# Kernel tuning notes

Measured on AMD Instinct MI355X. Metric: run time of the kernel, lower is better.

Reference implementation:

```python
import jax, jax.numpy as jnp
import numpy as np
import math

B, T, C = 2, 2048, 1024
H, DK, DV = 16, 64, 64


def setup_inputs() -> dict:
    key = jax.random.key(0)
    ks = jax.random.split(key, 5)
    # randw(*d) = randn(*d) / sqrt(d[-1])
    x = jax.random.normal(ks[0], (B, T, C), dtype=jnp.float32)
    w_q = jax.random.normal(ks[1], (H, DK, C), dtype=jnp.float32) / math.sqrt(C)
    w_k = jax.random.normal(ks[2], (H, DK, C), dtype=jnp.float32) / math.sqrt(C)
    w_v = jax.random.normal(ks[3], (H, DV, C), dtype=jnp.float32) / math.sqrt(C)
    w_o = jax.random.normal(ks[4], (H * DV, C), dtype=jnp.float32) / math.sqrt(C)
    return {"x": x, "w_q": w_q, "w_k": w_k, "w_v": w_v, "w_o": w_o}


def reference(x, w_q, w_k, w_v, w_o):
    # Full prefill: bs_q.first = 0, bs_q.nb = T, causal=True, dropout=0 (eval).
    dk = w_q.shape[1]
    q = jnp.einsum('ntc,hdc->nhtd', x, w_q)  # [B,H,T,DK]
    k = jnp.einsum('ntc,hdc->nhtd', x, w_k)  # [B,H,T,DK]
    v = jnp.einsum('ntc,hdc->nhtd', x, w_v)  # [B,H,T,DV]
    a = jnp.einsum('nhtd,nhsd->nhts', q, k) / jnp.sqrt(jnp.asarray(dk, x.dtype))
    # amm_generator: mask where query_idx < key_idx (strict upper triangle)
    t = a.shape[-1]
    mask = jnp.arange(t)[:, None] < jnp.arange(t)[None, :]  # [T,T] bool
    a = jnp.where(mask[None, None], jnp.asarray(-jnp.inf, a.dtype), a)
    a = jax.nn.softmax(a, axis=-1)
    y = jnp.einsum('nhts,nhsd->nthd', a, v)  # [B,T,H,DV]
    y = y.reshape(y.shape[0], y.shape[1], -1)  # [B,T,H*DV]
    return y @ w_o  # [B,T,C]
```

## Files before the change

### kernel.cpp

```cpp
#include <hip/hip_runtime.h>
#include <hip/hip_bf16.h>

#define B_ 2
#define T_ 2048
#define C_ 1024
#define H_ 16
#define D_ 64

typedef __attribute__((ext_vector_type(8))) short bf16x8;
typedef __attribute__((ext_vector_type(4))) float f32x4;
typedef __attribute__((ext_vector_type(8))) unsigned short u16x8;
typedef __attribute__((ext_vector_type(2))) unsigned int u32x2;
typedef __attribute__((ext_vector_type(4))) unsigned int u32x4;

__device__ __forceinline__ unsigned short bf1(float a) {
    __bf16 x = (__bf16)a;
    return __builtin_bit_cast(unsigned short, x);
}
__device__ __forceinline__ unsigned int pk2(float a, float b) {
    return (unsigned int)bf1(a) | ((unsigned int)bf1(b) << 16);
}
__device__ __forceinline__ float bf2f(unsigned short u) {
    union { unsigned int u; float f; } v; v.u = (unsigned int)u << 16;
    return v.f;
}

__device__ __forceinline__ void gll16(const void* g, void* l) {
    __builtin_amdgcn_global_load_lds(
        (const __attribute__((address_space(1))) unsigned int*)g,
        (__attribute__((address_space(3))) unsigned int*)l, 16, 0, 0);
}

__global__ __launch_bounds__(256) void prep_all(
    const float* __restrict__ x, const float* __restrict__ wq,
    const float* __restrict__ wk, const float* __restrict__ wv,
    unsigned short* __restrict__ xb, unsigned short* __restrict__ wb)
{
    const int bid = blockIdx.x, tid = threadIdx.x;
    if (bid < 1024) {
        const size_t i = ((size_t)bid * 256 + tid) * 16;
        float4 f0 = *reinterpret_cast<const float4*>(x + i);
        float4 f1 = *reinterpret_cast<const float4*>(x + i + 4);
        float4 f2 = *reinterpret_cast<const float4*>(x + i + 8);
        float4 f3 = *reinterpret_cast<const float4*>(x + i + 12);
        u32x4 a = {pk2(f0.x, f0.y), pk2(f0.z, f0.w), pk2(f1.x, f1.y), pk2(f1.z, f1.w)};
        u32x4 b = {pk2(f2.x, f2.y), pk2(f2.z, f2.w), pk2(f3.x, f3.y), pk2(f3.z, f3.w)};
        *reinterpret_cast<u32x4*>(xb + i) = a;
        *reinterpret_cast<u32x4*>(xb + i + 8) = b;
    } else {
        const int rb = (bid - 1024) * 4;
        const float* src = (rb < 1024) ? wq + (size_t)rb * 1024
                         : (rb < 2048) ? wk + (size_t)(rb - 1024) * 1024
                                       : wv + (size_t)(rb - 2048) * 1024;
        const float sc = (rb < 1024) ? 0.125f * 1.4426950408889634f : 1.0f;
        const float4* s4 = (const float4*)src;
        u32x2* d = (u32x2*)(wb + (size_t)rb * 1024);
#pragma unroll
        for (int k = 0; k < 4; k++) {
            float4 v = s4[k * 256 + tid];
            u32x2 w;
            w[0] = pk2(v.x * sc, v.y * sc);
            w[1] = pk2(v.z * sc, v.w * sc);
            d[k * 256 + tid] = w;
        }
    }
}

__global__ __launch_bounds__(256) void qkv_gemm(
    const unsigned short* __restrict__ xb, const unsigned short* __restrict__ wb,
    unsigned short* __restrict__ qkv)
{
    __shared__ __align__(16) unsigned short As[128 * 32];
    __shared__ __align__(16) unsigned short Bs[128 * 32];
    const int tid = threadIdx.x;
    const int lane = tid & 63, wave = tid >> 6;
    const int g = lane >> 4, c16 = lane & 15;
    const int xcd = blockIdx.x & 7, idx = blockIdx.x >> 3;
    const int bm = (xcd << 2) + idx / 24, bn = idx % 24;
    const int jbase = bn << 7;
    const int which = jbase >> 10;

    const int srow = lane >> 2, sch = (lane & 3) << 3;
    const unsigned short* asrc = xb + ((size_t)(bm << 7) + wave * 32 + srow) * C_ + sch;
    const unsigned short* bsrc = wb + ((size_t)(bn << 7) + wave * 32 + srow) * C_ + sch;

    f32x4 acc[4][4];
#pragma unroll
    for (int i = 0; i < 4; i++)
#pragma unroll
        for (int j = 0; j < 4; j++) acc[i][j] = (f32x4){0.f, 0.f, 0.f, 0.f};

    const int wm = (wave >> 1) << 6, wn = (wave & 1) << 6;

    for (int t = 0; t < 32; ++t) {
        const int k0 = t << 5;
        __syncthreads();
        gll16(asrc + k0,           &As[(wave * 32) << 5]);
        gll16(asrc + k0 + 16 * C_, &As[(wave * 32 + 16) << 5]);
        gll16(bsrc + k0,           &Bs[(wave * 32) << 5]);
        gll16(bsrc + k0 + 16 * C_, &Bs[(wave * 32 + 16) << 5]);
        __syncthreads();

        bf16x8 af[4], bfv[4];
#pragma unroll
        for (int m = 0; m < 4; m++)
            af[m] = *reinterpret_cast<const bf16x8*>(&As[((wm + m * 16 + c16) << 5) + g * 8]);
#pragma unroll
        for (int n = 0; n < 4; n++)
            bfv[n] = *reinterpret_cast<const bf16x8*>(&Bs[((wn + n * 16 + c16) << 5) + g * 8]);
#pragma unroll
        for (int m = 0; m < 4; m++)
#pragma unroll
            for (int n = 0; n < 4; n++)
                acc[m][n] = __builtin_amdgcn_mfma_f32_16x16x32_bf16(af[m], bfv[n], acc[m][n], 0, 0, 0);
    }

    if (which < 2) {
#pragma unroll
        for (int m = 0; m < 4; m++) {
            const int grow = (bm << 7) + wm + m * 16 + (g << 2);
#pragma unroll
            for (int n = 0; n < 4; n++) {
                const int jj = (jbase + wn + n * 16 + c16) & 1023;
                const int h = jj >> 6, d = jj & 63;
#pragma unroll
                for (int r = 0; r < 4; r++) {
                    const int row = grow + r;
                    const int b = row >> 11, t = row & 2047;
                    const size_t off = ((size_t)((which * B_ + b) * H_ + h) * T_ + t) * 64 + d;
                    qkv[off] = bf1(acc[m][n][r]);
                }
            }
        }
    } else {
#pragma unroll
        for (int m = 0; m < 4; m++) {
            const int grow = (bm << 7) + wm + m * 16 + (g << 2);
            const int b = grow >> 11, t = grow & 2047;
#pragma unroll
            for (int n = 0; n < 4; n++) {
                const int jj = (jbase + wn + n * 16 + c16) & 1023;
                const int h = jj >> 6, d = jj & 63;
                u32x2 w;
                w[0] = pk2(acc[m][n][0], acc[m][n][1]);
                w[1] = pk2(acc[m][n][2], acc[m][n][3]);
                const size_t off = ((size_t)((2 * B_ + b) * H_ + h) * 64 + d) * T_ + t;
                *reinterpret_cast<u32x2*>(&qkv[off]) = w;
            }
        }
    }
}

__global__ __launch_bounds__(256) void attn(
    const unsigned short* __restrict__ qkv,
    unsigned short* __restrict__ opA, unsigned short* __restrict__ opB,
    float* __restrict__ lbuf)
{
    __shared__ __align__(16) unsigned short Ks0[64 * 64], Ks1[64 * 64];
    __shared__ __align__(16) unsigned short Vt0[64 * 64], Vt1[64 * 64];
    __shared__ __align__(16) unsigned short Ps[4][16 * 64];
    const int tid = threadIdx.x, lane = tid & 63, wave = tid >> 6;
    const int g = lane >> 4, c16 = lane & 15;
    const int xs = blockIdx.x & 7;
    const int inner = blockIdx.x >> 3;
    const int qt = 15 - (inner >> 3);
    const int split = (inner >> 2) & 1;
    const int bh = (xs << 2) + (inner & 3);
    const int b = bh >> 4, h = bh & 15;
    const size_t headoff = (size_t)(b * H_ + h) * T_ * 64;
    const size_t QSZ = (size_t)B_ * H_ * T_ * 64;
    const unsigned short* qp = qkv + headoff;
    const unsigned short* kp = qkv + QSZ + headoff;
    const unsigned short* vTp = qkv + 2 * QSZ + headoff;

    const int h1 = qt + 1;
    const int itlo = split ? h1 : 0, ithi = split ? (2 * qt + 2) : h1;

    const int qb0 = (qt << 7) + wave * 16;
    const int qb1 = qb0 + 64;
    bf16x8 qf00, qf01, qf10, qf11;
    {
        const size_t r0 = (size_t)(qb0 + c16) * 64;
        const size_t r1 = (size_t)(qb1 + c16) * 64;
        qf00 = *reinterpret_cast<const bf16x8*>(qp + r0 + g * 8);
        qf01 = *reinterpret_cast<const bf16x8*>(qp + r0 + 32 + g * 8);
        qf10 = *reinterpret_cast<const bf16x8*>(qp + r1 + g * 8);
        qf11 = *reinterpret_cast<const bf16x8*>(qp + r1 + 32 + g * 8);
    }

    const bf16x8 ones = {0x3F80, 0x3F80, 0x3F80, 0x3F80, 0x3F80, 0x3F80, 0x3F80, 0x3F80};
    f32x4 lac0 = (f32x4){0.f, 0.f, 0.f, 0.f}, lac1 = (f32x4){0.f, 0.f, 0.f, 0.f};
    f32x4 acc0[4], acc1[4];
#pragma unroll
    for (int i = 0; i < 4; i++) {
        acc0[i] = (f32x4){0.f, 0.f, 0.f, 0.f};
        acc1[i] = (f32x4){0.f, 0.f, 0.f, 0.f};
    }

    const int sw = c16 & 7;
    const int rdo0 = (c16 << 6) + ((g ^ sw) << 3);
    const int rdo1 = (c16 << 6) + (((g + 4) ^ sw) << 3);
    const unsigned short* krA0 = Ks0 + rdo0;
    const unsigned short* krA1 = Ks0 + rdo1;
    const unsigned short* krB0 = Ks1 + rdo0;
    const unsigned short* krB1 = Ks1 + rdo1;
    const unsigned short* vrA0 = Vt0 + rdo0;
    const unsigned short* vrA1 = Vt0 + rdo1;
    const unsigned short* vrB0 = Vt1 + rdo0;
    const unsigned short* vrB1 = Vt1 + rdo1;
    const unsigned short* par0 = Ps[wave] + rdo0;
    const unsigned short* par1 = Ps[wave] + rdo1;
    unsigned short* pw[4];
#pragma unroll
    for (int f = 0; f < 4; f++)
        pw[f] = Ps[wave] + (c16 << 6)
              + (((((f << 1) + (g >> 1))) ^ sw) << 3) + ((g & 1) << 2);

    const int srow8 = lane >> 3;
    const int swc = ((lane & 7) ^ srow8) << 3;
    const unsigned short* ksrc = kp + (size_t)(wave * 16 + srow8) * 64 + swc;
    const unsigned short* vsrc = vTp + (size_t)(wave * 16 + srow8) * T_ + swc;

    auto stageTo = [&](unsigned short* kd, unsigned short* vd, int s0) {
#pragma unroll
        for (int i = 0; i < 2; i++) {
            gll16(ksrc + (size_t)(s0 + i * 8) * 64, kd + ((wave * 16 + i * 8) << 6));
            gll16(vsrc + s0 + (size_t)i * 8 * T_, vd + ((wave * 16 + i * 8) << 6));
        }
    };

    auto body = [&](const unsigned short* kr0, const unsigned short* kr1,
                    const unsigned short* vr0, const unsigned short* vr1, int s0) {
        f32x4 s0f[4], s1f[4];
#pragma unroll
        for (int f = 0; f < 4; f++) {
            s0f[f] = (f32x4){-16.f, -16.f, -16.f, -16.f};
            s1f[f] = (f32x4){-16.f, -16.f, -16.f, -16.f};
        }
        __builtin_amdgcn_s_setprio(1);
#pragma unroll
        for (int f = 0; f < 4; f++) {
            bf16x8 k0 = *reinterpret_cast<const bf16x8*>(kr0 + f * 1024);
            bf16x8 k1 = *reinterpret_cast<const bf16x8*>(kr1 + f * 1024);
            s0f[f] = __builtin_amdgcn_mfma_f32_16x16x32_bf16(k0, qf00, s0f[f], 0, 0, 0);
            s1f[f] = __builtin_amdgcn_mfma_f32_16x16x32_bf16(k0, qf10, s1f[f], 0, 0, 0);
            s0f[f] = __builtin_amdgcn_mfma_f32_16x16x32_bf16(k1, qf01, s0f[f], 0, 0, 0);
            s1f[f] = __builtin_amdgcn_mfma_f32_16x16x32_bf16(k1, qf11, s1f[f], 0, 0, 0);
        }
        __builtin_amdgcn_s_setprio(0);

        if (s0 + 63 > qb0) {
            const int qg = qb0 + c16;
#pragma unroll
            for (int f = 0; f < 4; f++)
#pragma unroll
                for (int r = 0; r < 4; r++)
                    if (s0 + f * 16 + g * 4 + r > qg) s0f[f][r] = -1e30f;
        }
        if (s0 + 63 > qb1) {
            const int qg = qb1 + c16;
#pragma unroll
            for (int f = 0; f < 4; f++)
#pragma unroll
                for (int r = 0; r < 4; r++)
                    if (s0 + f * 16 + g * 4 + r > qg) s1f[f][r] = -1e30f;
        }

        if (s0 <= qb0 + 15) {
#pragma unroll
            for (int f = 0; f < 4; f++)
#pragma unroll
                for (int r = 0; r < 4; r++)
                    s0f[f][r] = __builtin_amdgcn_exp2f(s0f[f][r]);
#pragma unroll
            for (int f = 0; f < 4; f++) {
                u32x2 w;
                w[0] = pk2(s0f[f][0], s0f[f][1]);
                w[1] = pk2(s0f[f][2], s0f[f][3]);
                *reinterpret_cast<u32x2*>(pw[f]) = w;
            }
            __builtin_amdgcn_s_setprio(1);
#pragma unroll
            for (int ks = 0; ks < 2; ks++) {
                bf16x8 pa = *reinterpret_cast<const bf16x8*>(ks ? par1 : par0);
                const unsigned short* vp = ks ? vr1 : vr0;
                lac0 = __builtin_amdgcn_mfma_f32_16x16x32_bf16(ones, pa, lac0, 0, 0, 0);
#pragma unroll
                for (int fd = 0; fd < 4; fd++) {
                    bf16x8 vf = *reinterpret_cast<const bf16x8*>(vp + fd * 1024);
                    acc0[fd] = __builtin_amdgcn_mfma_f32_16x16x32_bf16(vf, pa, acc0[fd], 0, 0, 0);
                }
            }
            __builtin_amdgcn_s_setprio(0);
        }

        {
#pragma unroll
            for (int f = 0; f < 4; f++)
#pragma unroll
                for (int r = 0; r < 4; r++)
                    s1f[f][r] = __builtin_amdgcn_exp2f(s1f[f][r]);
#pragma unroll
            for (int f = 0; f < 4; f++) {
                u32x2 w;
                w[0] = pk2(s1f[f][0], s1f[f][1]);
                w[1] = pk2(s1f[f][2], s1f[f][3]);
                *reinterpret_cast<u32x2*>(pw[f]) = w;
            }
            __builtin_amdgcn_s_setprio(1);
#pragma unroll
            for (int ks = 0; ks < 2; ks++) {
                bf16x8 pa = *reinterpret_cast<const bf16x8*>(ks ? par1 : par0);
                const unsigned short* vp = ks ? vr1 : vr0;
                lac1 = __builtin_amdgcn_mfma_f32_16x16x32_bf16(ones, pa, lac1, 0, 0, 0);
#pragma unroll
                for (int fd = 0; fd < 4; fd++) {
                    bf16x8 vf = *reinterpret_cast<const bf16x8*>(vp + fd * 1024);
                    acc1[fd] = __builtin_amdgcn_mfma_f32_16x16x32_bf16(vf, pa, acc1[fd], 0, 0, 0);
                }
            }
            __builtin_amdgcn_s_setprio(0);
        }
    };

    if (itlo < ithi) {
        stageTo(Ks0, Vt0, itlo << 6);
        int it = itlo;
        while (it + 2 <= ithi) {
            __syncthreads();
            stageTo(Ks1, Vt1, (it + 1) << 6);
            body(krA0, krA1, vrA0, vrA1, it << 6);
            __syncthreads();
            if (it + 2 < ithi) stageTo(Ks0, Vt0, (it + 2) << 6);
            body(krB0, krB1, vrB0, vrB1, (it + 1) << 6);
            it += 2;
        }
        if (it < ithi) {
            __syncthreads();
            body(krA0, krA1, vrA0, vrA1, it << 6);
        }
    }

    unsigned short* op = split ? opB : opA;
#pragma unroll
    for (int fd = 0; fd < 4; fd++) {
        u32x2 w0, w1;
        w0[0] = pk2(acc0[fd][0], acc0[fd][1]);
        w0[1] = pk2(acc0[fd][2], acc0[fd][3]);
        w1[0] = pk2(acc1[fd][0], acc1[fd][1]);
        w1[1] = pk2(acc1[fd][2], acc1[fd][3]);
        const size_t c0 = ((size_t)b * T_ + qb0 + c16) * 1024 + h * 64 + fd * 16 + g * 4;
        const size_t c1 = ((size_t)b * T_ + qb1 + c16) * 1024 + h * 64 + fd * 16 + g * 4;
        *reinterpret_cast<u32x2*>(&op[c0]) = w0;
        *reinterpret_cast<u32x2*>(&op[c1]) = w1;
    }
    if (lane < 16) {
        const size_t base = (size_t)split * (B_ * H_ * T_) + ((size_t)(b * H_ + h)) * T_;
        lbuf[base + qb0 + c16] = lac0[0];
        lbuf[base + qb1 + c16] = lac1[0];
    }
}

__global__ __launch_bounds__(256) void combine_wo(
    const unsigned short* __restrict__ opA, const unsigned short* __restrict__ opB,
    const float* __restrict__ lbuf, unsigned short* __restrict__ y,
    const float* __restrict__ wo, unsigned short* __restrict__ wt)
{
    __shared__ unsigned short tile[64][72];
    const int bid = blockIdx.x, tid = threadIdx.x;
    if (bid < 2048) {
        const size_t i = ((size_t)bid * 256 + tid) * 8;
        const int hh = (int)((i >> 6) & 15);
        const int t = (int)((i >> 10) & 2047);
        const int bb = (int)(i >> 21);
        const size_t li = ((size_t)(bb * H_ + hh)) * T_ + t;
        const float inv = 1.0f / (lbuf[li] + lbuf[(size_t)B_ * H_ * T_ + li]);
        u16x8 a = *reinterpret_cast<const u16x8*>(opA + i);
        u16x8 c = *reinterpret_cast<const u16x8*>(opB + i);
        unsigned short o[8];
#pragma unroll
        for (int j = 0; j < 8; j++) o[j] = bf1((bf2f(a[j]) + bf2f(c[j])) * inv);
        *reinterpret_cast<u16x8*>(y + i) = *reinterpret_cast<u16x8*>(o);
    } else {
        const int wb2 = bid - 2048;
        const int tk = (wb2 & 15) << 6, tn = (wb2 >> 4) << 6;
        const int r = tid >> 2, cb = (tid & 3) << 4;
#pragma unroll
        for (int j = 0; j < 4; j++) {
            float4 v = *reinterpret_cast<const float4*>(
                wo + (size_t)(tk + r) * 1024 + tn + cb + j * 4);
            u32x2 w;
            w[0] = pk2(v.x, v.y);
            w[1] = pk2(v.z, v.w);
            *reinterpret_cast<u32x2*>(&tile[r][cb + j * 4]) = w;
        }
        __syncthreads();
        unsigned short buf[16];
#pragma unroll
        for (int j = 0; j < 16; j++) buf[j] = tile[cb + j][r];
        unsigned short* dst = wt + (size_t)(tn + r) * 1024 + tk + cb;
        *reinterpret_cast<u16x8*>(dst) = *reinterpret_cast<u16x8*>(buf);
        *reinterpret_cast<u16x8*>(dst + 8) = *reinterpret_cast<u16x8*>(buf + 8);
    }
}

__global__ __launch_bounds__(256) void out_proj(
    const unsigned short* __restrict__ y, const unsigned short* __restrict__ wt,
    float* __restrict__ out)
{
    __shared__ __align__(16) unsigned short As[128 * 32];
    __shared__ __align__(16) unsigned short Bs[64 * 32];
    const int tid = threadIdx.x;
    const int lane = tid & 63, wave = tid >> 6;
    const int g = lane >> 4, c16 = lane & 15;
    const int xcd = blockIdx.x & 7, idx = blockIdx.x >> 3;
    const int bm = (xcd << 2) + (idx >> 4), bn = idx & 15;
    const int wm = (wave >> 1) << 6, wn = (wave & 1) << 5;

    const int srow = lane >> 2, sch = (lane & 3) << 3;
    const unsigned short* ysrc = y + ((size_t)(bm << 7) + wave * 32 + srow) * 1024 + sch;
    const unsigned short* wsrc = wt + ((size_t)(bn << 6) + wave * 16 + srow) * 1024 + sch;

    f32x4 acc[4][2];
#pragma unroll
    for (int i = 0; i < 4; i++)
#pragma unroll
        for (int j = 0; j < 2; j++) acc[i][j] = (f32x4){0.f, 0.f, 0.f, 0.f};

    for (int t = 0; t < 32; ++t) {
        const int k0 = t << 5;
        __syncthreads();
        gll16(ysrc + k0,             &As[(wave * 32) << 5]);
        gll16(ysrc + k0 + 16 * 1024, &As[(wave * 32 + 16) << 5]);
        gll16(wsrc + k0,             &Bs[(wave * 16) << 5]);
        __syncthreads();

        bf16x8 af[4], bfr[2];
#pragma unroll
        for (int m = 0; m < 4; m++)
            af[m] = *reinterpret_cast<const bf16x8*>(&As[((wm + m * 16 + c16) << 5) + g * 8]);
#pragma unroll
        for (int n = 0; n < 2; n++)
            bfr[n] = *reinterpret_cast<const bf16x8*>(&Bs[((wn + n * 16 + c16) << 5) + g * 8]);
#pragma unroll
        for (int m = 0; m < 4; m++)
#pragma unroll
            for (int n = 0; n < 2; n++)
                acc[m][n] = __builtin_amdgcn_mfma_f32_16x16x32_bf16(af[m], bfr[n], acc[m][n], 0, 0, 0);
    }

#pragma unroll
    for (int m = 0; m < 4; m++) {
        const int grow = (bm << 7) + wm + m * 16 + (g << 2);
#pragma unroll
        for (int n = 0; n < 2; n++) {
            const int gcol = (bn << 6) + wn + n * 16 + c16;
#pragma unroll
            for (int r = 0; r < 4; r++)
                out[(size_t)(grow + r) * 1024 + gcol] = acc[m][n][r];
        }
    }
}

extern "C" void kernel_launch(void* const* d_in, const int* in_sizes, int n_in,
                              void* d_out, int out_size, void* d_ws, size_t ws_size,
                              hipStream_t stream) {
    const float* x  = (const float*)d_in[0];
    const float* wq = (const float*)d_in[1];
    const float* wk = (const float*)d_in[2];
    const float* wv = (const float*)d_in[3];
    const float* wo = (const float*)d_in[4];
    float* out = (float*)d_out;

    unsigned short* wb   = (unsigned short*)d_ws;
    unsigned short* opB  = (unsigned short*)d_ws;
    unsigned short* y    = opB;
    unsigned short* qkv  = (unsigned short*)d_ws + (size_t)4 * 1024 * 1024;
    unsigned short* wt   = qkv;
    unsigned short* xb   = (unsigned short*)d_out;
    unsigned short* opA  = (unsigned short*)d_out;
    float* lbuf = (float*)((char*)d_out + (size_t)8 * 1024 * 1024);

    prep_all<<<dim3(1792), 256, 0, stream>>>(x, wq, wk, wv, xb, wb);
    qkv_gemm<<<dim3(768), 256, 0, stream>>>(xb, wb, qkv);
    attn<<<dim3(1024), 256, 0, stream>>>(qkv, opA, opB, lbuf);
    combine_wo<<<dim3(2048 + 256), 256, 0, stream>>>(opA, opB, lbuf, y, wo, wt);
    out_proj<<<dim3(512), 256, 0, stream>>>(y, wt, out);
}
```

Before: 108.5 us.

## Pair mirrored 64-row query tiles per block to balance causal attention work

```diff
diff --git a/kernel.cpp b/kernel.cpp
--- a/kernel.cpp
+++ b/kernel.cpp
@@ -163,7 +163,7 @@
     const int g = lane >> 4, c16 = lane & 15;
     const int xs = blockIdx.x & 7;
     const int inner = blockIdx.x >> 3;
-    const int qt = 15 - (inner >> 3);
+    const int p = inner >> 3;
     const int split = (inner >> 2) & 1;
     const int bh = (xs << 2) + (inner & 3);
     const int b = bh >> 4, h = bh & 15;
@@ -173,28 +173,30 @@
     const unsigned short* kp = qkv + QSZ + headoff;
     const unsigned short* vTp = qkv + 2 * QSZ + headoff;
 
-    const int h1 = qt + 1;
-    const int itlo = split ? h1 : 0, ithi = split ? (2 * qt + 2) : h1;
-
-    const int qb0 = (qt << 7) + wave * 16;
-    const int qb1 = qb0 + 64;
-    bf16x8 qf00, qf01, qf10, qf11;
+    const int tA = p, tB = 31 - p;
+    const int hs = (p >= 7) ? 8 : (15 - p);
+    const int itlo = split ? hs : 0;
+    const int ithi = split ? (tB + 1) : hs;
+
+    const int qbA = (tA << 6) + wave * 16;
+    const int qbB = (tB << 6) + wave * 16;
+    bf16x8 qfA0, qfA1, qfB0, qfB1;
     {
-        const size_t r0 = (size_t)(qb0 + c16) * 64;
-        const size_t r1 = (size_t)(qb1 + c16) * 64;
-        qf00 = *reinterpret_cast<const bf16x8*>(qp + r0 + g * 8);
-        qf01 = *reinterpret_cast<const bf16x8*>(qp + r0 + 32 + g * 8);
-        qf10 = *reinterpret_cast<const bf16x8*>(qp + r1 + g * 8);
-        qf11 = *reinterpret_cast<const bf16x8*>(qp + r1 + 32 + g * 8);
+        const size_t rA = (size_t)(qbA + c16) * 64;
+        const size_t rB = (size_t)(qbB + c16) * 64;
+        qfA0 = *reinterpret_cast<const bf16x8*>(qp + rA + g * 8);
+        qfA1 = *reinterpret_cast<const bf16x8*>(qp + rA + 32 + g * 8);
+        qfB0 = *reinterpret_cast<const bf16x8*>(qp + rB + g * 8);
+        qfB1 = *reinterpret_cast<const bf16x8*>(qp + rB + 32 + g * 8);
     }
 
     const bf16x8 ones = {0x3F80, 0x3F80, 0x3F80, 0x3F80, 0x3F80, 0x3F80, 0x3F80, 0x3F80};
-    f32x4 lac0 = (f32x4){0.f, 0.f, 0.f, 0.f}, lac1 = (f32x4){0.f, 0.f, 0.f, 0.f};
-    f32x4 acc0[4], acc1[4];
+    f32x4 lacA = (f32x4){0.f, 0.f, 0.f, 0.f}, lacB = (f32x4){0.f, 0.f, 0.f, 0.f};
+    f32x4 accA[4], accB[4];
 #pragma unroll
     for (int i = 0; i < 4; i++) {
-        acc0[i] = (f32x4){0.f, 0.f, 0.f, 0.f};
-        acc1[i] = (f32x4){0.f, 0.f, 0.f, 0.f};
+        accA[i] = (f32x4){0.f, 0.f, 0.f, 0.f};
+        accB[i] = (f32x4){0.f, 0.f, 0.f, 0.f};
     }
 
     const int sw = c16 & 7;
@@ -230,53 +232,83 @@
     };
 
     auto body = [&](const unsigned short* kr0, const unsigned short* kr1,
-                    const unsigned short* vr0, const unsigned short* vr1, int s0) {
-        f32x4 s0f[4], s1f[4];
+                    const unsigned short* vr0, const unsigned short* vr1, int it) {
+        const int s0 = it << 6;
+        const bool doA = (it <= tA);
+        f32x4 sA[4], sB[4];
 #pragma unroll
         for (int f = 0; f < 4; f++) {
-            s0f[f] = (f32x4){-16.f, -16.f, -16.f, -16.f};
-            s1f[f] = (f32x4){-16.f, -16.f, -16.f, -16.f};
+            sA[f] = (f32x4){-16.f, -16.f, -16.f, -16.f};
+            sB[f] = (f32x4){-16.f, -16.f, -16.f, -16.f};
         }
         __builtin_amdgcn_s_setprio(1);
 #pragma unroll
         for (int f = 0; f < 4; f++) {
             bf16x8 k0 = *reinterpret_cast<const bf16x8*>(kr0 + f * 1024);
             bf16x8 k1 = *reinterpret_cast<const bf16x8*>(kr1 + f * 1024);
-            s0f[f] = __builtin_amdgcn_mfma_f32_16x16x32_bf16(k0, qf00, s0f[f], 0, 0, 0);
-            s1f[f] = __builtin_amdgcn_mfma_f32_16x16x32_bf16(k0, qf10, s1f[f], 0, 0, 0);
-            s0f[f] = __builtin_amdgcn_mfma_f32_16x16x32_bf16(k1, qf01, s0f[f], 0, 0, 0);
-            s1f[f] = __builtin_amdgcn_mfma_f32_16x16x32_bf16(k1, qf11, s1f[f], 0, 0, 0);
+            sB[f] = __builtin_amdgcn_mfma_f32_16x16x32_bf16(k0, qfB0, sB[f], 0, 0, 0);
+            sB[f] = __builtin_amdgcn_mfma_f32_16x16x32_bf16(k1, qfB1, sB[f], 0, 0, 0);
+            if (doA) {
+                sA[f] = __builtin_amdgcn_mfma_f32_16x16x32_bf16(k0, qfA0, sA[f], 0, 0, 0);
+                sA[f] = __builtin_amdgcn_mfma_f32_16x16x32_bf16(k1, qfA1, sA[f], 0, 0, 0);
+            }
         }
         __builtin_amdgcn_s_setprio(0);
 
-        if (s0 + 63 > qb0) {
-            const int qg = qb0 + c16;
+        if (it == tB) {
+            const int qg = qbB + c16;
 #pragma unroll
             for (int f = 0; f < 4; f++)
 #pragma unroll
                 for (int r = 0; r < 4; r++)
-                    if (s0 + f * 16 + g * 4 + r > qg) s0f[f][r] = -1e30f;
-        }
-        if (s0 + 63 > qb1) {
-            const int qg = qb1 + c16;
+                    if (s0 + f * 16 + g * 4 + r > qg) sB[f][r] = -1e30f;
+        }
+
+#pragma unroll
+        for (int f = 0; f < 4; f++)
+#pragma unroll
+            for (int r = 0; r < 4; r++)
+                sB[f][r] = __builtin_amdgcn_exp2f(sB[f][r]);
+#pragma unroll
+        for (int f = 0; f < 4; f++) {
+            u32x2 w;
+            w[0] = pk2(sB[f][0], sB[f][1]);
+            w[1] = pk2(sB[f][2], sB[f][3]);
+            *reinterpret_cast<u32x2*>(pw[f]) = w;
+        }
+        __builtin_amdgcn_s_setprio(1);
+#pragma unroll
+        for (int ks = 0; ks < 2; ks++) {
+            bf16x8 pa = *reinterpret_cast<const bf16x8*>(ks ? par1 : par0);
+            const unsigned short* vp = ks ? vr1 : vr0;
+            lacB = __builtin_amdgcn_mfma_f32_16x16x32_bf16(ones, pa, lacB, 0, 0, 0);
+#pragma unroll
+            for (int fd = 0; fd < 4; fd++) {
+                bf16x8 vf = *reinterpret_cast<const bf16x8*>(vp + fd * 1024);
+                accB[fd] = __builtin_amdgcn_mfma_f32_16x16x32_bf16(vf, pa, accB[fd], 0, 0, 0);
+            }
+        }
+        __builtin_amdgcn_s_setprio(0);
+
+        if (doA) {
+            if (it == tA) {
+                const int qg = qbA + c16;
+#pragma unroll
+                for (int f = 0; f < 4; f++)
+#pragma unroll
+                    for (int r = 0; r < 4; r++)
+                        if (s0 + f * 16 + g * 4 + r > qg) sA[f][r] = -1e30f;
+            }
 #pragma unroll
             for (int f = 0; f < 4; f++)
 #pragma unroll
                 for (int r = 0; r < 4; r++)
-                    if (s0 + f * 16 + g * 4 + r > qg) s1f[f][r] = -1e30f;
-        }
-
-        if (s0 <= qb0 + 15) {
-#pragma unroll
-            for (int f = 0; f < 4; f++)
-#pragma unroll
-                for (int r = 0; r < 4; r++)
-                    s0f[f][r] = __builtin_amdgcn_exp2f(s0f[f][r]);
+                    sA[f][r] = __builtin_amdgcn_exp2f(sA[f][r]);
 #pragma unroll
             for (int f = 0; f < 4; f++) {
                 u32x2 w;
-                w[0] = pk2(s0f[f][0], s0f[f][1]);
-                w[1] = pk2(s0f[f][2], s0f[f][3]);
+                w[0] = pk2(sA[f][0], sA[f][1]);
+                w[1] = pk2(sA[f][2], sA[f][3]);
                 *reinterpret_cast<u32x2*>(pw[f]) = w;
             }
             __builtin_amdgcn_s_setprio(1);
@@ -284,39 +316,11 @@
             for (int ks = 0; ks < 2; ks++) {
                 bf16x8 pa = *reinterpret_cast<const bf16x8*>(ks ? par1 : par0);
                 const unsigned short* vp = ks ? vr1 : vr0;
-                lac0 = __builtin_amdgcn_mfma_f32_16x16x32_bf16(ones, pa, lac0, 0, 0, 0);
+                lacA = __builtin_amdgcn_mfma_f32_16x16x32_bf16(ones, pa, lacA, 0, 0, 0);
 #pragma unroll
                 for (int fd = 0; fd < 4; fd++) {
                     bf16x8 vf = *reinterpret_cast<const bf16x8*>(vp + fd * 1024);
-                    acc0[fd] = __builtin_amdgcn_mfma_f32_16x16x32_bf16(vf, pa, acc0[fd], 0, 0, 0);
-                }
-            }
-            __builtin_amdgcn_s_setprio(0);
-        }
-
-        {
-#pragma unroll
-            for (int f = 0; f < 4; f++)
-#pragma unroll
-                for (int r = 0; r < 4; r++)
-                    s1f[f][r] = __builtin_amdgcn_exp2f(s1f[f][r]);
-#pragma unroll
-            for (int f = 0; f < 4; f++) {
-                u32x2 w;
-                w[0] = pk2(s1f[f][0], s1f[f][1]);
-                w[1] = pk2(s1f[f][2], s1f[f][3]);
-                *reinterpret_cast<u32x2*>(pw[f]) = w;
-            }
-            __builtin_amdgcn_s_setprio(1);
-#pragma unroll
-            for (int ks = 0; ks < 2; ks++) {
-                bf16x8 pa = *reinterpret_cast<const bf16x8*>(ks ? par1 : par0);
-                const unsigned short* vp = ks ? vr1 : vr0;
-                lac1 = __builtin_amdgcn_mfma_f32_16x16x32_bf16(ones, pa, lac1, 0, 0, 0);
-#pragma unroll
-                for (int fd = 0; fd < 4; fd++) {
-                    bf16x8 vf = *reinterpret_cast<const bf16x8*>(vp + fd * 1024);
-                    acc1[fd] = __builtin_amdgcn_mfma_f32_16x16x32_bf16(vf, pa, acc1[fd], 0, 0, 0);
+                    accA[fd] = __builtin_amdgcn_mfma_f32_16x16x32_bf16(vf, pa, accA[fd], 0, 0, 0);
                 }
             }
             __builtin_amdgcn_s_setprio(0);
@@ -329,35 +333,35 @@
         while (it + 2 <= ithi) {
             __syncthreads();
             stageTo(Ks1, Vt1, (it + 1) << 6);
-            body(krA0, krA1, vrA0, vrA1, it << 6);
+            body(krA0, krA1, vrA0, vrA1, it);
             __syncthreads();
             if (it + 2 < ithi) stageTo(Ks0, Vt0, (it + 2) << 6);
-            body(krB0, krB1, vrB0, vrB1, (it + 1) << 6);
+            body(krB0, krB1, vrB0, vrB1, it + 1);
             it += 2;
         }
         if (it < ithi) {
             __syncthreads();
-            body(krA0, krA1, vrA0, vrA1, it << 6);
+            body(krA0, krA1, vrA0, vrA1, it);
         }
     }
 
     unsigned short* op = split ? opB : opA;
 #pragma unroll
     for (int fd = 0; fd < 4; fd++) {
-        u32x2 w0, w1;
-        w0[0] = pk2(acc0[fd][0], acc0[fd][1]);
-        w0[1] = pk2(acc0[fd][2], acc0[fd][3]);
-        w1[0] = pk2(acc1[fd][0], acc1[fd][1]);
-        w1[1] = pk2(acc1[fd][2], acc1[fd][3]);
-        const size_t c0 = ((size_t)b * T_ + qb0 + c16) * 1024 + h * 64 + fd * 16 + g * 4;
-        const size_t c1 = ((size_t)b * T_ + qb1 + c16) * 1024 + h * 64 + fd * 16 + g * 4;
-        *reinterpret_cast<u32x2*>(&op[c0]) = w0;
-        *reinterpret_cast<u32x2*>(&op[c1]) = w1;
+        u32x2 wA, wB;
+        wA[0] = pk2(accA[fd][0], accA[fd][1]);
+        wA[1] = pk2(accA[fd][2], accA[fd][3]);
+        wB[0] = pk2(accB[fd][0], accB[fd][1]);
+        wB[1] = pk2(accB[fd][2], accB[fd][3]);
+        const size_t cA = ((size_t)b * T_ + qbA + c16) * 1024 + h * 64 + fd * 16 + g * 4;
+        const size_t cB = ((size_t)b * T_ + qbB + c16) * 1024 + h * 64 + fd * 16 + g * 4;
+        *reinterpret_cast<u32x2*>(&op[cA]) = wA;
+        *reinterpret_cast<u32x2*>(&op[cB]) = wB;
     }
     if (lane < 16) {
         const size_t base = (size_t)split * (B_ * H_ * T_) + ((size_t)(b * H_ + h)) * T_;
-        lbuf[base + qb0 + c16] = lac0[0];
-        lbuf[base + qb1 + c16] = lac1[0];
+        lbuf[base + qbA + c16] = lacA[0];
+        lbuf[base + qbB + c16] = lacB[0];
     }
 }
 
```

Result: slower. 112.8 us (+4.0%).

## Triple-buffer LDS staging with explicit vmcnt waits in QKV GEMM and attention

Applied to the files above, without the earlier changes.

```diff
diff --git a/kernel.cpp b/kernel.cpp
--- a/kernel.cpp
+++ b/kernel.cpp
@@ -30,6 +30,9 @@
         (const __attribute__((address_space(1))) unsigned int*)g,
         (__attribute__((address_space(3))) unsigned int*)l, 16, 0, 0);
 }
+
+#define VM_WAIT4() asm volatile("s_waitcnt vmcnt(4)" ::: "memory")
+#define VM_WAIT0() asm volatile("s_waitcnt vmcnt(0)" ::: "memory")
 
 __global__ __launch_bounds__(256) void prep_all(
     const float* __restrict__ x, const float* __restrict__ wq,
@@ -70,8 +73,7 @@
     const unsigned short* __restrict__ xb, const unsigned short* __restrict__ wb,
     unsigned short* __restrict__ qkv)
 {
-    __shared__ __align__(16) unsigned short As[128 * 32];
-    __shared__ __align__(16) unsigned short Bs[128 * 32];
+    __shared__ __align__(16) unsigned short ABs[3][2][128 * 32];
     const int tid = threadIdx.x;
     const int lane = tid & 63, wave = tid >> 6;
     const int g = lane >> 4, c16 = lane & 15;
@@ -92,27 +94,36 @@
 
     const int wm = (wave >> 1) << 6, wn = (wave & 1) << 6;
 
+    auto stage = [&](int bi, int k0) {
+        gll16(asrc + k0,           &ABs[bi][0][(wave * 32) << 5]);
+        gll16(asrc + k0 + 16 * C_, &ABs[bi][0][(wave * 32 + 16) << 5]);
+        gll16(bsrc + k0,           &ABs[bi][1][(wave * 32) << 5]);
+        gll16(bsrc + k0 + 16 * C_, &ABs[bi][1][(wave * 32 + 16) << 5]);
+    };
+
+    stage(0, 0);
+    stage(1, 32);
+    int bi = 0;
     for (int t = 0; t < 32; ++t) {
-        const int k0 = t << 5;
-        __syncthreads();
-        gll16(asrc + k0,           &As[(wave * 32) << 5]);
-        gll16(asrc + k0 + 16 * C_, &As[(wave * 32 + 16) << 5]);
-        gll16(bsrc + k0,           &Bs[(wave * 32) << 5]);
-        gll16(bsrc + k0 + 16 * C_, &Bs[(wave * 32 + 16) << 5]);
-        __syncthreads();
-
+        if (t < 31) { VM_WAIT4(); } else { VM_WAIT0(); }
+        __builtin_amdgcn_s_barrier();
+        if (t + 2 < 32) stage(bi + 2 >= 3 ? bi - 1 : bi + 2, (t + 2) << 5);
+
+        const unsigned short* Ab = &ABs[bi][0][0];
+        const unsigned short* Bb = &ABs[bi][1][0];
         bf16x8 af[4], bfv[4];
 #pragma unroll
         for (int m = 0; m < 4; m++)
-            af[m] = *reinterpret_cast<const bf16x8*>(&As[((wm + m * 16 + c16) << 5) + g * 8]);
+            af[m] = *reinterpret_cast<const bf16x8*>(&Ab[((wm + m * 16 + c16) << 5) + g * 8]);
 #pragma unroll
         for (int n = 0; n < 4; n++)
-            bfv[n] = *reinterpret_cast<const bf16x8*>(&Bs[((wn + n * 16 + c16) << 5) + g * 8]);
+            bfv[n] = *reinterpret_cast<const bf16x8*>(&Bb[((wn + n * 16 + c16) << 5) + g * 8]);
 #pragma unroll
         for (int m = 0; m < 4; m++)
 #pragma unroll
             for (int n = 0; n < 4; n++)
                 acc[m][n] = __builtin_amdgcn_mfma_f32_16x16x32_bf16(af[m], bfv[n], acc[m][n], 0, 0, 0);
+        bi = (bi + 1 == 3) ? 0 : bi + 1;
     }
 
     if (which < 2) {
@@ -156,8 +167,7 @@
     unsigned short* __restrict__ opA, unsigned short* __restrict__ opB,
     float* __restrict__ lbuf)
 {
-    __shared__ __align__(16) unsigned short Ks0[64 * 64], Ks1[64 * 64];
-    __shared__ __align__(16) unsigned short Vt0[64 * 64], Vt1[64 * 64];
+    __shared__ __align__(16) unsigned short KV[3][2][64 * 64];
     __shared__ __align__(16) unsigned short Ps[4][16 * 64];
     const int tid = threadIdx.x, lane = tid & 63, wave = tid >> 6;
     const int g = lane >> 4, c16 = lane & 15;
@@ -200,14 +210,6 @@
     const int sw = c16 & 7;
     const int rdo0 = (c16 << 6) + ((g ^ sw) << 3);
     const int rdo1 = (c16 << 6) + (((g + 4) ^ sw) << 3);
-    const unsigned short* krA0 = Ks0 + rdo0;
-    const unsigned short* krA1 = Ks0 + rdo1;
-    const unsigned short* krB0 = Ks1 + rdo0;
-    const unsigned short* krB1 = Ks1 + rdo1;
-    const unsigned short* vrA0 = Vt0 + rdo0;
-    const unsigned short* vrA1 = Vt0 + rdo1;
-    const unsigned short* vrB0 = Vt1 + rdo0;
-    const unsigned short* vrB1 = Vt1 + rdo1;
     const unsigned short* par0 = Ps[wave] + rdo0;
     const unsigned short* par1 = Ps[wave] + rdo1;
     unsigned short* pw[4];
@@ -221,16 +223,23 @@
     const unsigned short* ksrc = kp + (size_t)(wave * 16 + srow8) * 64 + swc;
     const unsigned short* vsrc = vTp + (size_t)(wave * 16 + srow8) * T_ + swc;
 
-    auto stageTo = [&](unsigned short* kd, unsigned short* vd, int s0) {
+    auto stageTo = [&](int bi, int s0) {
 #pragma unroll
         for (int i = 0; i < 2; i++) {
-            gll16(ksrc + (size_t)(s0 + i * 8) * 64, kd + ((wave * 16 + i * 8) << 6));
-            gll16(vsrc + s0 + (size_t)i * 8 * T_, vd + ((wave * 16 + i * 8) << 6));
+            gll16(ksrc + (size_t)(s0 + i * 8) * 64, &KV[bi][0][(wave * 16 + i * 8) << 6]);
+            gll16(vsrc + s0 + (size_t)i * 8 * T_, &KV[bi][1][(wave * 16 + i * 8) << 6]);
         }
     };
 
-    auto body = [&](const unsigned short* kr0, const unsigned short* kr1,
-                    const unsigned short* vr0, const unsigned short* vr1, int s0) {
+    auto body = [&](int bi, int it) {
+        const int s0 = it << 6;
+        const unsigned short* kb = &KV[bi][0][0];
+        const unsigned short* vb = &KV[bi][1][0];
+        const unsigned short* kr0 = kb + rdo0;
+        const unsigned short* kr1 = kb + rdo1;
+        const unsigned short* vr0 = vb + rdo0;
+        const unsigned short* vr1 = vb + rdo1;
+
         f32x4 s0f[4], s1f[4];
 #pragma unroll
         for (int f = 0; f < 4; f++) {
@@ -323,22 +332,15 @@
         }
     };
 
-    if (itlo < ithi) {
-        stageTo(Ks0, Vt0, itlo << 6);
-        int it = itlo;
-        while (it + 2 <= ithi) {
-            __syncthreads();
-            stageTo(Ks1, Vt1, (it + 1) << 6);
-            body(krA0, krA1, vrA0, vrA1, it << 6);
-            __syncthreads();
-            if (it + 2 < ithi) stageTo(Ks0, Vt0, (it + 2) << 6);
-            body(krB0, krB1, vrB0, vrB1, (it + 1) << 6);
-            it += 2;
-        }
-        if (it < ithi) {
-            __syncthreads();
-            body(krA0, krA1, vrA0, vrA1, it << 6);
-        }
+    stageTo(0, itlo << 6);
+    if (itlo + 1 < ithi) stageTo(1, (itlo + 1) << 6);
+    int bi = 0;
+    for (int it = itlo; it < ithi; ++it) {
+        if (it + 1 < ithi) { VM_WAIT4(); } else { VM_WAIT0(); }
+        __builtin_amdgcn_s_barrier();
+        if (it + 2 < ithi) stageTo(bi + 2 >= 3 ? bi - 1 : bi + 2, (it + 2) << 6);
+        body(bi, it);
+        bi = (bi + 1 == 3) ? 0 : bi + 1;
     }
 
     unsigned short* op = split ? opB : opA;
```

After: 115.3 us. 6.2% more time.
